# Kernel tuning notes

Hardware: AMD Instinct MI355X
Metric: run time of the kernel (lower is better)

Reference implementation:

```python
import jax, jax.numpy as jnp
import numpy as np

N_NODES = 100000
DROP_P = 0.2


def _degree_norm(idx, n):
    deg = jax.ops.segment_sum(jnp.ones_like(idx, dtype=jnp.float32), idx, num_segments=n)
    return jnp.maximum(deg, 1.0) ** -0.5


def gcn_layer(x, src, dst, W, b, n):
    # DGL GraphConv, norm='both', in_feats > out_feats so weight is applied first.
    norm_src = _degree_norm(src, n)  # out-degree^{-1/2}
    norm_dst = _degree_norm(dst, n)  # in-degree^{-1/2}
    h = (x * norm_src[:, None]) @ W            # [N, d_out]
    agg = jax.ops.segment_sum(h[src], dst, num_segments=n)  # gather-scatter over edges
    return agg * norm_dst[:, None] + b


def setup_inputs() -> dict:
    key = jax.random.key(0)
    k = jax.random.split(key, 5)
    x = jax.random.normal(k[0], (N_NODES, 256), dtype=jnp.float32)
    edge_index = jax.random.randint(k[1], (2, 1600000), 0, N_NODES, dtype=jnp.int64)
    W1 = jax.random.normal(k[2], (256, 128), dtype=jnp.float32) * (1.0 / np.sqrt(256))
    b1 = jnp.zeros((128,), dtype=jnp.float32)
    W2 = jax.random.normal(k[3], (128, 47), dtype=jnp.float32) * (1.0 / np.sqrt(128))
    b2 = jnp.zeros((47,), dtype=jnp.float32)
    return {"x": x, "edge_index": edge_index, "W1": W1, "b1": b1, "W2": W2, "b2": b2}


def reference(x, edge_index, W1, b1, W2, b2):
    src, dst = edge_index[0], edge_index[1]
    n = x.shape[0]
    # CRD: GraphConv -> relu -> dropout (F.dropout default training=True; fixed mask)
    h = gcn_layer(x, src, dst, W1, b1, n)
    h = jax.nn.relu(h)
    keep = jax.random.bernoulli(jax.random.key(42), 1.0 - DROP_P, h.shape)
    h = jnp.where(keep, h / (1.0 - DROP_P), 0.0)
    # CLS: GraphConv -> log_softmax over class dim
    out = gcn_layer(h, src, dst, W2, b2, n)
    return jax.nn.log_softmax(out, axis=-1)
```

## Files before the change

kernel.cpp:

```cpp
#include <hip/hip_runtime.h>
#include <math.h>


#define NF0 256
#define NF1 128
#define NC  47
#define CB  1024

typedef __attribute__((ext_vector_type(8))) short bfrag;
typedef __attribute__((ext_vector_type(4))) float f32x4;

__device__ __forceinline__ unsigned short f2bf(float f) {
  unsigned u = __float_as_uint(f);
  return (unsigned short)((u + 0x7fffu + ((u >> 16) & 1u)) >> 16);
}
__device__ __forceinline__ unsigned pack2bf(float a, float b) {
  return (unsigned)f2bf(a) | ((unsigned)f2bf(b) << 16);
}
__device__ __forceinline__ float bf2f(unsigned short b) {
  return __uint_as_float((unsigned)b << 16);
}
__device__ __forceinline__ float bflo(unsigned v) { return __uint_as_float(v << 16); }
__device__ __forceinline__ float bfhi(unsigned v) { return __uint_as_float(v & 0xffff0000u); }

__device__ __forceinline__ unsigned rotl_(unsigned x, int n) {
  return (x << n) | (x >> (32 - n));
}
__device__ __forceinline__ void threefry2x32_(unsigned x0, unsigned x1,
                                              unsigned& o0, unsigned& o1) {
  const unsigned k0 = 0u, k1 = 42u;
  const unsigned k2 = k0 ^ k1 ^ 0x1BD11BDAu;
  x0 += k0; x1 += k1;
  x0+=x1; x1=rotl_(x1,13); x1^=x0;
  x0+=x1; x1=rotl_(x1,15); x1^=x0;
  x0+=x1; x1=rotl_(x1,26); x1^=x0;
  x0+=x1; x1=rotl_(x1, 6); x1^=x0;
  x0+=k1; x1+=k2+1u;
  x0+=x1; x1=rotl_(x1,17); x1^=x0;
  x0+=x1; x1=rotl_(x1,29); x1^=x0;
  x0+=x1; x1=rotl_(x1,16); x1^=x0;
  x0+=x1; x1=rotl_(x1,24); x1^=x0;
  x0+=k2; x1+=k0+2u;
  x0+=x1; x1=rotl_(x1,13); x1^=x0;
  x0+=x1; x1=rotl_(x1,15); x1^=x0;
  x0+=x1; x1=rotl_(x1,26); x1^=x0;
  x0+=x1; x1=rotl_(x1, 6); x1^=x0;
  x0+=k0; x1+=k1+3u;
  x0+=x1; x1=rotl_(x1,17); x1^=x0;
  x0+=x1; x1=rotl_(x1,29); x1^=x0;
  x0+=x1; x1=rotl_(x1,16); x1^=x0;
  x0+=x1; x1=rotl_(x1,24); x1^=x0;
  x0+=k1; x1+=k2+4u;
  x0+=x1; x1=rotl_(x1,13); x1^=x0;
  x0+=x1; x1=rotl_(x1,15); x1^=x0;
  x0+=x1; x1=rotl_(x1,26); x1^=x0;
  x0+=x1; x1=rotl_(x1, 6); x1^=x0;
  x0+=k2; x1+=k0+5u;
  o0 = x0; o1 = x1;
}
__device__ __forceinline__ float dropout_mul(int j) {
  unsigned o0, o1;
  threefry2x32_(0u, (unsigned)j, o0, o1);
  unsigned bits = o0 ^ o1;
  float u = __uint_as_float((bits >> 9) | 0x3f800000u) - 1.0f;
  return (u < 0.8f) ? 1.25f : 0.0f;
}


__global__ __launch_bounds__(256) void k_chist(const int* __restrict__ ei, int E,
                                               int nbk,
                                               unsigned* __restrict__ bCntD,
                                               unsigned* __restrict__ bCntS) {
  __shared__ unsigned hd[128], hs[128];
  for (int i = threadIdx.x; i < 128; i += 256) { hd[i] = 0; hs[i] = 0; }
  __syncthreads();
  for (int e = blockIdx.x * 256 + threadIdx.x; e < E; e += gridDim.x * 256) {
    int s = ei[e], d = ei[E + e];
    atomicAdd(&hs[s >> 10], 1u);
    atomicAdd(&hd[d >> 10], 1u);
  }
  __syncthreads();
  for (int i = threadIdx.x; i < nbk; i += 256) {
    if (hd[i]) atomicAdd(&bCntD[i], hd[i]);
    if (hs[i]) atomicAdd(&bCntS[i], hs[i]);
  }
}

__global__ void k_cscan(const unsigned* __restrict__ bCntD,
                        const unsigned* __restrict__ bCntS,
                        unsigned* __restrict__ bOffD, unsigned* __restrict__ bOffS,
                        unsigned* __restrict__ curD, unsigned* __restrict__ curS,
                        unsigned* __restrict__ off, int nbk, int N, int E) {
  if (threadIdx.x == 0) {
    unsigned a = 0, b = 0;
    for (int i = 0; i < nbk; i++) {
      bOffD[i] = a; curD[i] = a; a += bCntD[i];
      bOffS[i] = b; curS[i] = b; b += bCntS[i];
    }
    bOffD[nbk] = a; bOffS[nbk] = b;
    off[N] = (unsigned)E;
  }
}

__global__ __launch_bounds__(256) void k_cscatter(const int* __restrict__ ei, int E,
                                                  unsigned* __restrict__ curD,
                                                  unsigned* __restrict__ curS,
                                                  unsigned* __restrict__ pd,
                                                  unsigned short* __restrict__ ps) {
  __shared__ unsigned hd[128], hs[128];
  __shared__ unsigned baseD[128], baseS[128];
  int per = (E + gridDim.x - 1) / gridDim.x;
  int e0 = blockIdx.x * per;
  int e1 = min(e0 + per, E);
  for (int i = threadIdx.x; i < 128; i += 256) { hd[i] = 0; hs[i] = 0; }
  __syncthreads();
  for (int e = e0 + threadIdx.x; e < e1; e += 256) {
    int s = ei[e], d = ei[E + e];
    atomicAdd(&hs[s >> 10], 1u);
    atomicAdd(&hd[d >> 10], 1u);
  }
  __syncthreads();
  for (int i = threadIdx.x; i < 128; i += 256) {
    baseD[i] = hd[i] ? atomicAdd(&curD[i], hd[i]) : 0u;
    baseS[i] = hs[i] ? atomicAdd(&curS[i], hs[i]) : 0u;
    hd[i] = 0; hs[i] = 0;
  }
  __syncthreads();
  for (int e = e0 + threadIdx.x; e < e1; e += 256) {
    int s = ei[e], d = ei[E + e];
    int bd = d >> 10, bs = s >> 10;
    unsigned pD = baseD[bd] + atomicAdd(&hd[bd], 1u);
    unsigned pS = baseS[bs] + atomicAdd(&hs[bs], 1u);
    pd[pD] = ((unsigned)(d & (CB - 1)) << 17) | (unsigned)s;
    ps[pS] = (unsigned short)(s & (CB - 1));
  }
}

__global__ __launch_bounds__(256) void k_fcsr(const unsigned* __restrict__ bOffD,
                                              const unsigned* __restrict__ pd,
                                              unsigned* __restrict__ off,
                                              unsigned* __restrict__ deg_dst, int N,
                                              int* __restrict__ csr) {
  __shared__ unsigned cnt[CB];
  __shared__ unsigned part[256];
  const int b = blockIdx.x, t = threadIdx.x;
  const unsigned lo = bOffD[b], hi = bOffD[b + 1];
  const int base = b << 10;
  for (int i = t; i < CB; i += 256) cnt[i] = 0;
  __syncthreads();
  for (unsigned j = lo + t; j < hi; j += 256) atomicAdd(&cnt[pd[j] >> 17], 1u);
  __syncthreads();
  unsigned c0 = cnt[4*t], c1 = cnt[4*t+1], c2 = cnt[4*t+2], c3 = cnt[4*t+3];
  unsigned tsum = c0 + c1 + c2 + c3;
  part[t] = tsum;
  __syncthreads();
  #pragma unroll
  for (int o = 1; o < 256; o <<= 1) {
    unsigned u = (t >= o) ? part[t - o] : 0u;
    __syncthreads();
    part[t] += u;
    __syncthreads();
  }
  unsigned e0 = part[t] - tsum;
  unsigned p0 = e0, p1 = e0 + c0, p2 = p1 + c1, p3 = p2 + c2;
  int n0 = base + 4 * t;
  if (n0 + 0 < N) { off[n0 + 0] = lo + p0; deg_dst[n0 + 0] = c0; }
  if (n0 + 1 < N) { off[n0 + 1] = lo + p1; deg_dst[n0 + 1] = c1; }
  if (n0 + 2 < N) { off[n0 + 2] = lo + p2; deg_dst[n0 + 2] = c2; }
  if (n0 + 3 < N) { off[n0 + 3] = lo + p3; deg_dst[n0 + 3] = c3; }
  __syncthreads();
  cnt[4*t] = p0; cnt[4*t+1] = p1; cnt[4*t+2] = p2; cnt[4*t+3] = p3;
  __syncthreads();
  for (unsigned j = lo + t; j < hi; j += 256) {
    unsigned v = pd[j];
    unsigned pos = atomicAdd(&cnt[v >> 17], 1u);
    csr[lo + pos] = (int)(v & 0x1FFFFu);
  }
}

__global__ __launch_bounds__(256) void k_fhist(const unsigned* __restrict__ bOffS,
                                               const unsigned short* __restrict__ ps,
                                               unsigned* __restrict__ deg_src, int N) {
  __shared__ unsigned cnt[CB];
  const int b = blockIdx.x, t = threadIdx.x;
  const unsigned lo = bOffS[b], hi = bOffS[b + 1];
  const int base = b << 10;
  for (int i = t; i < CB; i += 256) cnt[i] = 0;
  __syncthreads();
  for (unsigned j = lo + t; j < hi; j += 256) atomicAdd(&cnt[ps[j]], 1u);
  __syncthreads();
  for (int i = t; i < CB; i += 256)
    if (base + i < N) deg_src[base + i] = cnt[i];
}

__global__ __launch_bounds__(256) void k_norm(float* __restrict__ buf, int n2) {
  int i = blockIdx.x * 256 + threadIdx.x;
  if (i < n2) {
    unsigned d = ((const unsigned*)buf)[i];
    float df = (float)(d < 1u ? 1u : d);
    buf[i] = 1.0f / sqrtf(df);
  }
}

__global__ __launch_bounds__(256) void k_wcvt(const float* __restrict__ W1,
                                              const float* __restrict__ W2,
                                              unsigned* __restrict__ W1t32,
                                              unsigned short* __restrict__ W2t) {
  int i = blockIdx.x * 256 + threadIdx.x;
  if (i < 128 * 128) {
    int n = i >> 7, kp = i & 127;
    int k = kp << 1;
    W1t32[i] = pack2bf(W1[(size_t)k * NF1 + n], W1[(size_t)(k + 1) * NF1 + n]);
  } else if (i < 128 * 128 + 48 * 128) {
    int j = i - 128 * 128;
    int f = j >> 7, k = j & 127;
    W2t[j] = (f < NC) ? f2bf(W2[(size_t)k * NC + f]) : (unsigned short)0;
  }
}

__global__ __launch_bounds__(256) void k_gemm1(const float* __restrict__ x,
                                               const unsigned* __restrict__ W1t32,
                                               const float* __restrict__ norm_src,
                                               unsigned short* __restrict__ h1, int N) {
  __shared__ unsigned As[128][20];
  __shared__ unsigned Bs[128][20];
  const int m0 = blockIdx.x * 128;
  const int t = threadIdx.x;
  const int lane = t & 63, wid = t >> 6;
  const int fr = lane & 15, ko = (lane >> 4) * 8;

  f32x4 acc[2][8];
  #pragma unroll
  for (int r = 0; r < 2; r++)
    #pragma unroll
    for (int c = 0; c < 8; c++) acc[r][c] = (f32x4){0.f, 0.f, 0.f, 0.f};

  const int sr = t >> 1;
  const int shw = (t & 1) * 8;

  for (int k0 = 0; k0 < NF0; k0 += 32) {
    {
      unsigned w[8];
      int gm = m0 + sr;
      if (gm < N) {
        const float* p = x + (size_t)gm * NF0 + k0 + shw * 2;
        #pragma unroll
        for (int q = 0; q < 4; q++) {
          float4 v = *(const float4*)(p + q * 4);
          w[2*q]   = pack2bf(v.x, v.y);
          w[2*q+1] = pack2bf(v.z, v.w);
        }
      } else {
        #pragma unroll
        for (int q = 0; q < 8; q++) w[q] = 0u;
      }
      *(uint4*)&As[sr][shw]     = make_uint4(w[0], w[1], w[2], w[3]);
      *(uint4*)&As[sr][shw + 4] = make_uint4(w[4], w[5], w[6], w[7]);
    }
    {
      const unsigned* pb = W1t32 + (size_t)sr * (NF0 / 2) + (k0 >> 1) + shw;
      *(uint4*)&Bs[sr][shw]     = *(const uint4*)pb;
      *(uint4*)&Bs[sr][shw + 4] = *(const uint4*)(pb + 4);
    }
    __syncthreads();
    const unsigned short* As16 = (const unsigned short*)&As[0][0];
    const unsigned short* Bs16 = (const unsigned short*)&Bs[0][0];
    #pragma unroll
    for (int r = 0; r < 2; r++) {
      bfrag a = *(const bfrag*)(As16 + (size_t)(wid * 32 + r * 16 + fr) * 40 + ko);
      #pragma unroll
      for (int c = 0; c < 8; c++) {
        bfrag b = *(const bfrag*)(Bs16 + (size_t)(c * 16 + fr) * 40 + ko);
        acc[r][c] = __builtin_amdgcn_mfma_f32_16x16x32_bf16(a, b, acc[r][c], 0, 0, 0);
      }
    }
    __syncthreads();
  }

  #pragma unroll
  for (int r = 0; r < 2; r++) {
    int rbase = m0 + wid * 32 + r * 16 + (lane >> 4) * 4;
    float ns[4];
    #pragma unroll
    for (int g = 0; g < 4; g++) ns[g] = (rbase + g < N) ? norm_src[rbase + g] : 0.f;
    #pragma unroll
    for (int c = 0; c < 8; c++) {
      int col = c * 16 + fr;
      #pragma unroll
      for (int g = 0; g < 4; g++) {
        int row = rbase + g;
        if (row < N) h1[(size_t)row * NF1 + col] = f2bf(acc[r][c][g] * ns[g]);
      }
    }
  }
}

__global__ __launch_bounds__(256) void k_gather1(const unsigned* __restrict__ off,
                                                 const int* __restrict__ csr,
                                                 const unsigned short* __restrict__ h1,
                                                 const float* __restrict__ norm_dst,
                                                 const float* __restrict__ norm_src,
                                                 const float* __restrict__ b1,
                                                 unsigned short* __restrict__ h2, int N) {
  int node = (blockIdx.x * 256 + threadIdx.x) >> 6;
  int lane = threadIdx.x & 63;
  if (node >= N) return;
  unsigned j = off[node], e1 = off[node + 1];
  int f = lane << 1;
  float ax = 0.f, ay = 0.f;
  for (; j + 4 <= e1; j += 4) {
    int s0 = csr[j], s1 = csr[j+1], s2 = csr[j+2], s3 = csr[j+3];
    unsigned v0 = *(const unsigned*)(h1 + (size_t)s0 * NF1 + f);
    unsigned v1 = *(const unsigned*)(h1 + (size_t)s1 * NF1 + f);
    unsigned v2 = *(const unsigned*)(h1 + (size_t)s2 * NF1 + f);
    unsigned v3 = *(const unsigned*)(h1 + (size_t)s3 * NF1 + f);
    ax += (bflo(v0) + bflo(v1)) + (bflo(v2) + bflo(v3));
    ay += (bfhi(v0) + bfhi(v1)) + (bfhi(v2) + bfhi(v3));
  }
  for (; j < e1; j++) {
    unsigned v = *(const unsigned*)(h1 + (size_t)csr[j] * NF1 + f);
    ax += bflo(v); ay += bfhi(v);
  }
  float nd = norm_dst[node], ns = norm_src[node];
  float2 bb = *(const float2*)(b1 + f);
  float v0 = fmaxf(ax * nd + bb.x, 0.f);
  float v1 = fmaxf(ay * nd + bb.y, 0.f);
  int jf = node * NF1 + f;
  v0 *= dropout_mul(jf) * ns;
  v1 *= dropout_mul(jf + 1) * ns;
  *(unsigned*)(h2 + (size_t)node * NF1 + f) = pack2bf(v0, v1);
}

__global__ __launch_bounds__(256) void k_gemm2(const unsigned short* __restrict__ h2,
                                               const unsigned short* __restrict__ W2t,
                                               unsigned short* __restrict__ g, int N) {
  __shared__ float hs[64][132];
  __shared__ float w2t[48][132];
  const int m0 = blockIdx.x * 64;
  const int t = threadIdx.x;
  #pragma unroll
  for (int l = t; l < 64 * 16; l += 256) {
    int r = l >> 4, c8 = (l & 15) << 3;
    int gm = m0 + r;
    float f[8];
    if (gm < N) {
      uint4 v = *(const uint4*)(h2 + (size_t)gm * NF1 + c8);
      f[0]=bflo(v.x); f[1]=bfhi(v.x); f[2]=bflo(v.y); f[3]=bfhi(v.y);
      f[4]=bflo(v.z); f[5]=bfhi(v.z); f[6]=bflo(v.w); f[7]=bfhi(v.w);
    } else {
      #pragma unroll
      for (int q = 0; q < 8; q++) f[q] = 0.f;
    }
    *(float4*)&hs[r][c8]     = make_float4(f[0], f[1], f[2], f[3]);
    *(float4*)&hs[r][c8 + 4] = make_float4(f[4], f[5], f[6], f[7]);
  }
  for (int l = t; l < 48 * 128; l += 256) {
    int n = l >> 7, k = l & 127;
    w2t[n][k] = bf2f(W2t[l]);
  }
  __syncthreads();
  const int fg = t & 15, mg = t >> 4;
  const int f0 = fg * 3, mt = mg * 4;
  float acc[4][3] = {{0.f}};
  for (int k = 0; k < NF1; k += 4) {
    float4 a[4], b[3];
    #pragma unroll
    for (int i = 0; i < 4; i++) a[i] = *(float4*)&hs[mt + i][k];
    #pragma unroll
    for (int j = 0; j < 3; j++) b[j] = *(float4*)&w2t[f0 + j][k];
    #pragma unroll
    for (int i = 0; i < 4; i++)
      #pragma unroll
      for (int j = 0; j < 3; j++)
        acc[i][j] += a[i].x*b[j].x + a[i].y*b[j].y + a[i].z*b[j].z + a[i].w*b[j].w;
  }
  #pragma unroll
  for (int i = 0; i < 4; i++) {
    int gm = m0 + mt + i;
    if (gm < N) {
      #pragma unroll
      for (int j = 0; j < 3; j++)
        g[(size_t)gm * 48 + f0 + j] = f2bf(acc[i][j]);
    }
  }
}

__global__ __launch_bounds__(256) void k_gather2(const unsigned* __restrict__ off,
                                                 const int* __restrict__ csr,
                                                 const unsigned short* __restrict__ g,
                                                 const float* __restrict__ norm_dst,
                                                 const float* __restrict__ b2,
                                                 float* __restrict__ out, int N) {
  int node = (blockIdx.x * 256 + threadIdx.x) >> 6;
  int lane = threadIdx.x & 63;
  if (node >= N) return;
  unsigned j = off[node], e1 = off[node + 1];
  float acc = 0.f;
  for (; j + 4 <= e1; j += 4) {
    int s0 = csr[j], s1 = csr[j+1], s2 = csr[j+2], s3 = csr[j+3];
    if (lane < 48) {
      float a0 = bf2f(g[(size_t)s0 * 48 + lane]);
      float a1 = bf2f(g[(size_t)s1 * 48 + lane]);
      float a2 = bf2f(g[(size_t)s2 * 48 + lane]);
      float a3 = bf2f(g[(size_t)s3 * 48 + lane]);
      acc += (a0 + a1) + (a2 + a3);
    }
  }
  for (; j < e1; j++) {
    if (lane < 48) acc += bf2f(g[(size_t)csr[j] * 48 + lane]);
  }
  float nd = norm_dst[node];
  float vr = 0.f, m = -INFINITY;
  if (lane < NC) {
    vr = acc * nd + b2[lane];
    m = vr;
  }
  #pragma unroll
  for (int o = 32; o; o >>= 1) m = fmaxf(m, __shfl_xor(m, o));
  float ex = (lane < NC) ? expf(vr - m) : 0.f;
  #pragma unroll
  for (int o = 32; o; o >>= 1) ex += __shfl_xor(ex, o);
  float ls = logf(ex);
  if (lane < NC) out[(size_t)node * NC + lane] = vr - m - ls;
}

extern "C" void kernel_launch(void* const* d_in, const int* in_sizes, int n_in,
                              void* d_out, int out_size, void* d_ws, size_t ws_size,
                              hipStream_t stream) {
  const float* x  = (const float*)d_in[0];
  const int*   ei = (const int*)d_in[1];
  const float* W1 = (const float*)d_in[2];
  const float* b1 = (const float*)d_in[3];
  const float* W2 = (const float*)d_in[4];
  const float* b2 = (const float*)d_in[5];
  float* out = (float*)d_out;

  const int N = in_sizes[0] / NF0;
  const int E = in_sizes[1] / 2;
  const int nbk = (N + CB - 1) / CB;

  unsigned* ws = (unsigned*)d_ws;
  size_t o = 0;
  auto alloc = [&](size_t elems) { size_t p = o; o += (elems + 3) & ~(size_t)3; return p; };
  unsigned* deg_src = ws + alloc(N);
  unsigned* deg_dst = ws + alloc(N);
  unsigned* off     = ws + alloc(N + 1);
  unsigned* bCntD   = ws + alloc(128);
  unsigned* bCntS   = ws + alloc(128);
  unsigned* bOffD   = ws + alloc(132);
  unsigned* bOffS   = ws + alloc(132);
  unsigned* curD    = ws + alloc(128);
  unsigned* curS    = ws + alloc(128);
  unsigned* pd      = ws + alloc(E);
  unsigned short* ps = (unsigned short*)(ws + alloc(E / 2));
  int*      csr     = (int*)(ws + alloc(E));
  unsigned* W1t32   = ws + alloc(128 * 128);
  unsigned short* W2t = (unsigned short*)(ws + alloc(48 * 128 / 2));
  unsigned short* h1  = (unsigned short*)(ws + alloc((size_t)N * NF1 / 2));
  size_t need_h2 = (o + (size_t)N * NF1 / 2) * 4;
  unsigned short* h2 = (ws_size >= need_h2)
                           ? (unsigned short*)(ws + alloc((size_t)N * NF1 / 2))
                           : (unsigned short*)d_in[0];
  unsigned short* g = h1;

  hipMemsetAsync(bCntD, 0, 256 * sizeof(unsigned), stream);

  k_chist<<<256, 256, 0, stream>>>(ei, E, nbk, bCntD, bCntS);
  k_cscan<<<1, 64, 0, stream>>>(bCntD, bCntS, bOffD, bOffS, curD, curS, off, nbk, N, E);
  k_cscatter<<<256, 256, 0, stream>>>(ei, E, curD, curS, pd, ps);
  k_fcsr<<<nbk, 256, 0, stream>>>(bOffD, pd, off, deg_dst, N, csr);
  k_fhist<<<nbk, 256, 0, stream>>>(bOffS, ps, deg_src, N);
  k_norm<<<(2 * N + 255) / 256, 256, 0, stream>>>((float*)deg_src, 2 * N);
  k_wcvt<<<(128 * 128 + 48 * 128 + 255) / 256, 256, 0, stream>>>(W1, W2, W1t32, W2t);
  k_gemm1<<<(N + 127) / 128, 256, 0, stream>>>(x, W1t32, (const float*)deg_src, h1, N);
  k_gather1<<<((size_t)N * 64 + 255) / 256, 256, 0, stream>>>(
      off, csr, h1, (const float*)deg_dst, (const float*)deg_src, b1, h2, N);
  k_gemm2<<<(N + 63) / 64, 256, 0, stream>>>(h2, W2t, g, N);
  k_gather2<<<((size_t)N * 64 + 255) / 256, 256, 0, stream>>>(
      off, csr, g, (const float*)deg_dst, b2, out, N);
}
```

Before: 513.2 us.

## Fuse preprocessing kernels and merge layer-1 gather with layer-2 GEMM

```diff
diff --git a/kernel.cpp b/kernel.cpp
--- a/kernel.cpp
+++ b/kernel.cpp
@@ -17,11 +17,11 @@
 __device__ __forceinline__ unsigned pack2bf(float a, float b) {
   return (unsigned)f2bf(a) | ((unsigned)f2bf(b) << 16);
 }
+__device__ __forceinline__ float bflo(unsigned v) { return __uint_as_float(v << 16); }
+__device__ __forceinline__ float bfhi(unsigned v) { return __uint_as_float(v & 0xffff0000u); }
 __device__ __forceinline__ float bf2f(unsigned short b) {
   return __uint_as_float((unsigned)b << 16);
 }
-__device__ __forceinline__ float bflo(unsigned v) { return __uint_as_float(v << 16); }
-__device__ __forceinline__ float bfhi(unsigned v) { return __uint_as_float(v & 0xffff0000u); }
 
 __device__ __forceinline__ unsigned rotl_(unsigned x, int n) {
   return (x << n) | (x >> (32 - n));
@@ -70,11 +70,29 @@
 __global__ __launch_bounds__(256) void k_chist(const int* __restrict__ ei, int E,
                                                int nbk,
                                                unsigned* __restrict__ bCntD,
-                                               unsigned* __restrict__ bCntS) {
+                                               unsigned* __restrict__ bCntS,
+                                               const float* __restrict__ W1,
+                                               const float* __restrict__ W2,
+                                               unsigned* __restrict__ W1t32,
+                                               unsigned* __restrict__ W2t32) {
+  if (blockIdx.x >= 256) {
+    int i = (blockIdx.x - 256) * 256 + threadIdx.x;
+    if (i < 128 * 128) {
+      int n = i >> 7, k = (i & 127) << 1;
+      W1t32[i] = pack2bf(W1[(size_t)k * NF1 + n], W1[(size_t)(k + 1) * NF1 + n]);
+    } else if (i < 128 * 128 + 48 * 64) {
+      int j = i - 128 * 128;
+      int f = j >> 6, k = (j & 63) << 1;
+      float a = (f < NC) ? W2[(size_t)k * NC + f] : 0.f;
+      float c = (f < NC) ? W2[(size_t)(k + 1) * NC + f] : 0.f;
+      W2t32[j] = pack2bf(a, c);
+    }
+    return;
+  }
   __shared__ unsigned hd[128], hs[128];
   for (int i = threadIdx.x; i < 128; i += 256) { hd[i] = 0; hs[i] = 0; }
   __syncthreads();
-  for (int e = blockIdx.x * 256 + threadIdx.x; e < E; e += gridDim.x * 256) {
+  for (int e = blockIdx.x * 256 + threadIdx.x; e < E; e += 256 * 256) {
     int s = ei[e], d = ei[E + e];
     atomicAdd(&hs[s >> 10], 1u);
     atomicAdd(&hd[d >> 10], 1u);
@@ -86,47 +104,53 @@
   }
 }
 
-__global__ void k_cscan(const unsigned* __restrict__ bCntD,
-                        const unsigned* __restrict__ bCntS,
-                        unsigned* __restrict__ bOffD, unsigned* __restrict__ bOffS,
-                        unsigned* __restrict__ curD, unsigned* __restrict__ curS,
-                        unsigned* __restrict__ off, int nbk, int N, int E) {
-  if (threadIdx.x == 0) {
-    unsigned a = 0, b = 0;
-    for (int i = 0; i < nbk; i++) {
-      bOffD[i] = a; curD[i] = a; a += bCntD[i];
-      bOffS[i] = b; curS[i] = b; b += bCntS[i];
-    }
-    bOffD[nbk] = a; bOffS[nbk] = b;
-    off[N] = (unsigned)E;
-  }
-}
-
 __global__ __launch_bounds__(256) void k_cscatter(const int* __restrict__ ei, int E,
+                                                  const unsigned* __restrict__ bCntD,
+                                                  const unsigned* __restrict__ bCntS,
                                                   unsigned* __restrict__ curD,
                                                   unsigned* __restrict__ curS,
                                                   unsigned* __restrict__ pd,
-                                                  unsigned short* __restrict__ ps) {
+                                                  unsigned short* __restrict__ ps,
+                                                  int nbk) {
   __shared__ unsigned hd[128], hs[128];
   __shared__ unsigned baseD[128], baseS[128];
+  __shared__ unsigned sc[256];
+  const int t = threadIdx.x;
   int per = (E + gridDim.x - 1) / gridDim.x;
   int e0 = blockIdx.x * per;
   int e1 = min(e0 + per, E);
-  for (int i = threadIdx.x; i < 128; i += 256) { hd[i] = 0; hs[i] = 0; }
-  __syncthreads();
-  for (int e = e0 + threadIdx.x; e < e1; e += 256) {
+  unsigned orig = (t < 128) ? ((t < nbk) ? bCntD[t] : 0u)
+                            : (((t - 128) < nbk) ? bCntS[t - 128] : 0u);
+  sc[t] = orig;
+  if (t < 128) { hd[t] = 0; hs[t] = 0; }
+  __syncthreads();
+  for (int e = e0 + t; e < e1; e += 256) {
     int s = ei[e], d = ei[E + e];
     atomicAdd(&hs[s >> 10], 1u);
     atomicAdd(&hd[d >> 10], 1u);
   }
   __syncthreads();
-  for (int i = threadIdx.x; i < 128; i += 256) {
-    baseD[i] = hd[i] ? atomicAdd(&curD[i], hd[i]) : 0u;
-    baseS[i] = hs[i] ? atomicAdd(&curS[i], hs[i]) : 0u;
-    hd[i] = 0; hs[i] = 0;
-  }
-  __syncthreads();
-  for (int e = e0 + threadIdx.x; e < e1; e += 256) {
+  #pragma unroll
+  for (int o = 1; o < 128; o <<= 1) {
+    unsigned u = ((t & 127) >= o) ? sc[t - o] : 0u;
+    __syncthreads();
+    sc[t] += u;
+    __syncthreads();
+  }
+  if (t < 128) {
+    unsigned excl = sc[t] - orig;
+    unsigned h = hd[t];
+    baseD[t] = excl + (h ? atomicAdd(&curD[t], h) : 0u);
+    hd[t] = 0;
+  } else {
+    int i = t - 128;
+    unsigned excl = sc[t] - orig;
+    unsigned h = hs[i];
+    baseS[i] = excl + (h ? atomicAdd(&curS[i], h) : 0u);
+    hs[i] = 0;
+  }
+  __syncthreads();
+  for (int e = e0 + t; e < e1; e += 256) {
     int s = ei[e], d = ei[E + e];
     int bd = d >> 10, bs = s >> 10;
     unsigned pD = baseD[bd] + atomicAdd(&hd[bd], 1u);
@@ -136,85 +160,78 @@
   }
 }
 
-__global__ __launch_bounds__(256) void k_fcsr(const unsigned* __restrict__ bOffD,
+__global__ __launch_bounds__(256) void k_fine(const unsigned* __restrict__ bCntD,
+                                              const unsigned* __restrict__ bCntS,
                                               const unsigned* __restrict__ pd,
+                                              const unsigned short* __restrict__ ps,
                                               unsigned* __restrict__ off,
-                                              unsigned* __restrict__ deg_dst, int N,
-                                              int* __restrict__ csr) {
+                                              float* __restrict__ norm_dst,
+                                              float* __restrict__ norm_src,
+                                              int* __restrict__ csr,
+                                              int N, int E, int nbk) {
   __shared__ unsigned cnt[CB];
   __shared__ unsigned part[256];
-  const int b = blockIdx.x, t = threadIdx.x;
-  const unsigned lo = bOffD[b], hi = bOffD[b + 1];
+  __shared__ unsigned sc[256];
+  const int t = threadIdx.x;
+  const bool isD = (int)blockIdx.x < nbk;
+  const int b = isD ? (int)blockIdx.x : ((int)blockIdx.x - nbk);
+  unsigned orig = (t < 128) ? ((t < nbk) ? bCntD[t] : 0u)
+                            : (((t - 128) < nbk) ? bCntS[t - 128] : 0u);
+  sc[t] = orig;
+  __syncthreads();
+  #pragma unroll
+  for (int o = 1; o < 128; o <<= 1) {
+    unsigned u = ((t & 127) >= o) ? sc[t - o] : 0u;
+    __syncthreads();
+    sc[t] += u;
+    __syncthreads();
+  }
+  const int idx = isD ? b : (128 + b);
+  const unsigned hi = sc[idx];
+  const unsigned lo = hi - (isD ? bCntD[b] : bCntS[b]);
   const int base = b << 10;
   for (int i = t; i < CB; i += 256) cnt[i] = 0;
   __syncthreads();
-  for (unsigned j = lo + t; j < hi; j += 256) atomicAdd(&cnt[pd[j] >> 17], 1u);
-  __syncthreads();
-  unsigned c0 = cnt[4*t], c1 = cnt[4*t+1], c2 = cnt[4*t+2], c3 = cnt[4*t+3];
-  unsigned tsum = c0 + c1 + c2 + c3;
-  part[t] = tsum;
-  __syncthreads();
-  #pragma unroll
-  for (int o = 1; o < 256; o <<= 1) {
-    unsigned u = (t >= o) ? part[t - o] : 0u;
-    __syncthreads();
-    part[t] += u;
-    __syncthreads();
-  }
-  unsigned e0 = part[t] - tsum;
-  unsigned p0 = e0, p1 = e0 + c0, p2 = p1 + c1, p3 = p2 + c2;
-  int n0 = base + 4 * t;
-  if (n0 + 0 < N) { off[n0 + 0] = lo + p0; deg_dst[n0 + 0] = c0; }
-  if (n0 + 1 < N) { off[n0 + 1] = lo + p1; deg_dst[n0 + 1] = c1; }
-  if (n0 + 2 < N) { off[n0 + 2] = lo + p2; deg_dst[n0 + 2] = c2; }
-  if (n0 + 3 < N) { off[n0 + 3] = lo + p3; deg_dst[n0 + 3] = c3; }
-  __syncthreads();
-  cnt[4*t] = p0; cnt[4*t+1] = p1; cnt[4*t+2] = p2; cnt[4*t+3] = p3;
-  __syncthreads();
-  for (unsigned j = lo + t; j < hi; j += 256) {
-    unsigned v = pd[j];
-    unsigned pos = atomicAdd(&cnt[v >> 17], 1u);
-    csr[lo + pos] = (int)(v & 0x1FFFFu);
-  }
-}
-
-__global__ __launch_bounds__(256) void k_fhist(const unsigned* __restrict__ bOffS,
-                                               const unsigned short* __restrict__ ps,
-                                               unsigned* __restrict__ deg_src, int N) {
-  __shared__ unsigned cnt[CB];
-  const int b = blockIdx.x, t = threadIdx.x;
-  const unsigned lo = bOffS[b], hi = bOffS[b + 1];
-  const int base = b << 10;
-  for (int i = t; i < CB; i += 256) cnt[i] = 0;
-  __syncthreads();
-  for (unsigned j = lo + t; j < hi; j += 256) atomicAdd(&cnt[ps[j]], 1u);
-  __syncthreads();
-  for (int i = t; i < CB; i += 256)
-    if (base + i < N) deg_src[base + i] = cnt[i];
-}
-
-__global__ __launch_bounds__(256) void k_norm(float* __restrict__ buf, int n2) {
-  int i = blockIdx.x * 256 + threadIdx.x;
-  if (i < n2) {
-    unsigned d = ((const unsigned*)buf)[i];
-    float df = (float)(d < 1u ? 1u : d);
-    buf[i] = 1.0f / sqrtf(df);
-  }
-}
-
-__global__ __launch_bounds__(256) void k_wcvt(const float* __restrict__ W1,
-                                              const float* __restrict__ W2,
-                                              unsigned* __restrict__ W1t32,
-                                              unsigned short* __restrict__ W2t) {
-  int i = blockIdx.x * 256 + threadIdx.x;
-  if (i < 128 * 128) {
-    int n = i >> 7, kp = i & 127;
-    int k = kp << 1;
-    W1t32[i] = pack2bf(W1[(size_t)k * NF1 + n], W1[(size_t)(k + 1) * NF1 + n]);
-  } else if (i < 128 * 128 + 48 * 128) {
-    int j = i - 128 * 128;
-    int f = j >> 7, k = j & 127;
-    W2t[j] = (f < NC) ? f2bf(W2[(size_t)k * NC + f]) : (unsigned short)0;
+  if (isD) {
+    for (unsigned j = lo + t; j < hi; j += 256) atomicAdd(&cnt[pd[j] >> 17], 1u);
+    __syncthreads();
+    unsigned c0 = cnt[4*t], c1 = cnt[4*t+1], c2 = cnt[4*t+2], c3 = cnt[4*t+3];
+    unsigned tsum = c0 + c1 + c2 + c3;
+    part[t] = tsum;
+    __syncthreads();
+    #pragma unroll
+    for (int o = 1; o < 256; o <<= 1) {
+      unsigned u = (t >= o) ? part[t - o] : 0u;
+      __syncthreads();
+      part[t] += u;
+      __syncthreads();
+    }
+    unsigned e0 = part[t] - tsum;
+    unsigned p0 = e0, p1 = e0 + c0, p2 = p1 + c1, p3 = p2 + c2;
+    int n0 = base + 4 * t;
+    if (n0 + 0 < N) { off[n0+0] = lo + p0; norm_dst[n0+0] = 1.0f / sqrtf((float)(c0 < 1u ? 1u : c0)); }
+    if (n0 + 1 < N) { off[n0+1] = lo + p1; norm_dst[n0+1] = 1.0f / sqrtf((float)(c1 < 1u ? 1u : c1)); }
+    if (n0 + 2 < N) { off[n0+2] = lo + p2; norm_dst[n0+2] = 1.0f / sqrtf((float)(c2 < 1u ? 1u : c2)); }
+    if (n0 + 3 < N) { off[n0+3] = lo + p3; norm_dst[n0+3] = 1.0f / sqrtf((float)(c3 < 1u ? 1u : c3)); }
+    if (b == nbk - 1 && t == 0) off[N] = (unsigned)E;
+    __syncthreads();
+    cnt[4*t] = p0; cnt[4*t+1] = p1; cnt[4*t+2] = p2; cnt[4*t+3] = p3;
+    __syncthreads();
+    for (unsigned j = lo + t; j < hi; j += 256) {
+      unsigned v = pd[j];
+      unsigned pos = atomicAdd(&cnt[v >> 17], 1u);
+      csr[lo + pos] = (int)(v & 0x1FFFFu);
+    }
+  } else {
+    for (unsigned j = lo + t; j < hi; j += 256) atomicAdd(&cnt[ps[j]], 1u);
+    __syncthreads();
+    for (int i = t; i < CB; i += 256) {
+      int n = base + i;
+      if (n < N) {
+        unsigned c = cnt[i];
+        norm_src[n] = 1.0f / sqrtf((float)(c < 1u ? 1u : c));
+      }
+    }
   }
 }
 
@@ -295,92 +312,83 @@
   }
 }
 
-__global__ __launch_bounds__(256) void k_gather1(const unsigned* __restrict__ off,
-                                                 const int* __restrict__ csr,
-                                                 const unsigned short* __restrict__ h1,
-                                                 const float* __restrict__ norm_dst,
-                                                 const float* __restrict__ norm_src,
-                                                 const float* __restrict__ b1,
-                                                 unsigned short* __restrict__ h2, int N) {
-  int node = (blockIdx.x * 256 + threadIdx.x) >> 6;
-  int lane = threadIdx.x & 63;
-  if (node >= N) return;
-  unsigned j = off[node], e1 = off[node + 1];
-  int f = lane << 1;
-  float ax = 0.f, ay = 0.f;
-  for (; j + 4 <= e1; j += 4) {
-    int s0 = csr[j], s1 = csr[j+1], s2 = csr[j+2], s3 = csr[j+3];
-    unsigned v0 = *(const unsigned*)(h1 + (size_t)s0 * NF1 + f);
-    unsigned v1 = *(const unsigned*)(h1 + (size_t)s1 * NF1 + f);
-    unsigned v2 = *(const unsigned*)(h1 + (size_t)s2 * NF1 + f);
-    unsigned v3 = *(const unsigned*)(h1 + (size_t)s3 * NF1 + f);
-    ax += (bflo(v0) + bflo(v1)) + (bflo(v2) + bflo(v3));
-    ay += (bfhi(v0) + bfhi(v1)) + (bfhi(v2) + bfhi(v3));
-  }
-  for (; j < e1; j++) {
-    unsigned v = *(const unsigned*)(h1 + (size_t)csr[j] * NF1 + f);
-    ax += bflo(v); ay += bfhi(v);
-  }
-  float nd = norm_dst[node], ns = norm_src[node];
-  float2 bb = *(const float2*)(b1 + f);
-  float v0 = fmaxf(ax * nd + bb.x, 0.f);
-  float v1 = fmaxf(ay * nd + bb.y, 0.f);
-  int jf = node * NF1 + f;
-  v0 *= dropout_mul(jf) * ns;
-  v1 *= dropout_mul(jf + 1) * ns;
-  *(unsigned*)(h2 + (size_t)node * NF1 + f) = pack2bf(v0, v1);
-}
-
-__global__ __launch_bounds__(256) void k_gemm2(const unsigned short* __restrict__ h2,
-                                               const unsigned short* __restrict__ W2t,
-                                               unsigned short* __restrict__ g, int N) {
-  __shared__ float hs[64][132];
-  __shared__ float w2t[48][132];
+#define G2PAD 70
+__global__ __launch_bounds__(256) void k_g1g2(const unsigned* __restrict__ off,
+                                              const int* __restrict__ csr,
+                                              const unsigned short* __restrict__ h1,
+                                              const float* __restrict__ norm_dst,
+                                              const float* __restrict__ norm_src,
+                                              const float* __restrict__ b1,
+                                              const unsigned* __restrict__ W2t32,
+                                              unsigned short* __restrict__ g, int N) {
+  __shared__ unsigned hsb[64 * G2PAD];
+  const int t = threadIdx.x;
   const int m0 = blockIdx.x * 64;
-  const int t = threadIdx.x;
-  #pragma unroll
-  for (int l = t; l < 64 * 16; l += 256) {
-    int r = l >> 4, c8 = (l & 15) << 3;
-    int gm = m0 + r;
-    float f[8];
-    if (gm < N) {
-      uint4 v = *(const uint4*)(h2 + (size_t)gm * NF1 + c8);
-      f[0]=bflo(v.x); f[1]=bfhi(v.x); f[2]=bflo(v.y); f[3]=bfhi(v.y);
-      f[4]=bflo(v.z); f[5]=bfhi(v.z); f[6]=bflo(v.w); f[7]=bfhi(v.w);
-    } else {
-      #pragma unroll
-      for (int q = 0; q < 8; q++) f[q] = 0.f;
-    }
-    *(float4*)&hs[r][c8]     = make_float4(f[0], f[1], f[2], f[3]);
-    *(float4*)&hs[r][c8 + 4] = make_float4(f[4], f[5], f[6], f[7]);
-  }
-  for (int l = t; l < 48 * 128; l += 256) {
-    int n = l >> 7, k = l & 127;
-    w2t[n][k] = bf2f(W2t[l]);
-  }
-  __syncthreads();
+  const int lane = t & 63, wid = t >> 6;
+  const int f = lane << 1;
+
+  for (int nn = 0; nn < 16; nn++) {
+    int lrow = wid * 16 + nn;
+    int node = m0 + lrow;
+    if (node >= N) break;
+    unsigned j = off[node], e1 = off[node + 1];
+    float ax = 0.f, ay = 0.f;
+    for (; j + 4 <= e1; j += 4) {
+      int s0 = csr[j], s1 = csr[j+1], s2 = csr[j+2], s3 = csr[j+3];
+      unsigned v0 = *(const unsigned*)(h1 + (size_t)s0 * NF1 + f);
+      unsigned v1 = *(const unsigned*)(h1 + (size_t)s1 * NF1 + f);
+      unsigned v2 = *(const unsigned*)(h1 + (size_t)s2 * NF1 + f);
+      unsigned v3 = *(const unsigned*)(h1 + (size_t)s3 * NF1 + f);
+      ax += (bflo(v0) + bflo(v1)) + (bflo(v2) + bflo(v3));
+      ay += (bfhi(v0) + bfhi(v1)) + (bfhi(v2) + bfhi(v3));
+    }
+    for (; j < e1; j++) {
+      unsigned v = *(const unsigned*)(h1 + (size_t)csr[j] * NF1 + f);
+      ax += bflo(v); ay += bfhi(v);
+    }
+    float nd = norm_dst[node], ns = norm_src[node];
+    float2 bb = *(const float2*)(b1 + f);
+    float v0 = fmaxf(ax * nd + bb.x, 0.f);
+    float v1 = fmaxf(ay * nd + bb.y, 0.f);
+    int jf = node * NF1 + f;
+    v0 *= dropout_mul(jf) * ns;
+    v1 *= dropout_mul(jf + 1) * ns;
+    hsb[lrow * G2PAD + lane] = pack2bf(v0, v1);
+  }
+  __syncthreads();
+
   const int fg = t & 15, mg = t >> 4;
   const int f0 = fg * 3, mt = mg * 4;
   float acc[4][3] = {{0.f}};
   for (int k = 0; k < NF1; k += 4) {
-    float4 a[4], b[3];
-    #pragma unroll
-    for (int i = 0; i < 4; i++) a[i] = *(float4*)&hs[mt + i][k];
-    #pragma unroll
-    for (int j = 0; j < 3; j++) b[j] = *(float4*)&w2t[f0 + j][k];
+    float a[4][4];
+    #pragma unroll
+    for (int i = 0; i < 4; i++) {
+      uint2 u = *(const uint2*)&hsb[(mt + i) * G2PAD + (k >> 1)];
+      a[i][0] = bflo(u.x); a[i][1] = bfhi(u.x);
+      a[i][2] = bflo(u.y); a[i][3] = bfhi(u.y);
+    }
+    float bv[3][4];
+    #pragma unroll
+    for (int jj = 0; jj < 3; jj++) {
+      uint2 u = *(const uint2*)(W2t32 + (size_t)(f0 + jj) * 64 + (k >> 1));
+      bv[jj][0] = bflo(u.x); bv[jj][1] = bfhi(u.x);
+      bv[jj][2] = bflo(u.y); bv[jj][3] = bfhi(u.y);
+    }
     #pragma unroll
     for (int i = 0; i < 4; i++)
       #pragma unroll
-      for (int j = 0; j < 3; j++)
-        acc[i][j] += a[i].x*b[j].x + a[i].y*b[j].y + a[i].z*b[j].z + a[i].w*b[j].w;
+      for (int jj = 0; jj < 3; jj++)
+        acc[i][jj] += a[i][0]*bv[jj][0] + a[i][1]*bv[jj][1]
+                    + a[i][2]*bv[jj][2] + a[i][3]*bv[jj][3];
   }
   #pragma unroll
   for (int i = 0; i < 4; i++) {
     int gm = m0 + mt + i;
     if (gm < N) {
       #pragma unroll
-      for (int j = 0; j < 3; j++)
-        g[(size_t)gm * 48 + f0 + j] = f2bf(acc[i][j]);
+      for (int jj = 0; jj < 3; jj++)
+        g[(size_t)gm * 48 + f0 + jj] = f2bf(acc[i][jj]);
     }
   }
 }
@@ -442,40 +450,36 @@
   unsigned* ws = (unsigned*)d_ws;
   size_t o = 0;
   auto alloc = [&](size_t elems) { size_t p = o; o += (elems + 3) & ~(size_t)3; return p; };
-  unsigned* deg_src = ws + alloc(N);
-  unsigned* deg_dst = ws + alloc(N);
-  unsigned* off     = ws + alloc(N + 1);
-  unsigned* bCntD   = ws + alloc(128);
-  unsigned* bCntS   = ws + alloc(128);
-  unsigned* bOffD   = ws + alloc(132);
-  unsigned* bOffS   = ws + alloc(132);
-  unsigned* curD    = ws + alloc(128);
-  unsigned* curS    = ws + alloc(128);
-  unsigned* pd      = ws + alloc(E);
+  float*    norm_src = (float*)(ws + alloc(N));
+  float*    norm_dst = (float*)(ws + alloc(N));
+  unsigned* off      = ws + alloc(N + 1);
+  unsigned* bCntD    = ws + alloc(128);
+  unsigned* bCntS    = ws + alloc(128);
+  unsigned* curD     = ws + alloc(128);
+  unsigned* curS     = ws + alloc(128);
+  unsigned* pd       = ws + alloc(E);
   unsigned short* ps = (unsigned short*)(ws + alloc(E / 2));
-  int*      csr     = (int*)(ws + alloc(E));
-  unsigned* W1t32   = ws + alloc(128 * 128);
-  unsigned short* W2t = (unsigned short*)(ws + alloc(48 * 128 / 2));
-  unsigned short* h1  = (unsigned short*)(ws + alloc((size_t)N * NF1 / 2));
-  size_t need_h2 = (o + (size_t)N * NF1 / 2) * 4;
-  unsigned short* h2 = (ws_size >= need_h2)
-                           ? (unsigned short*)(ws + alloc((size_t)N * NF1 / 2))
-                           : (unsigned short*)d_in[0];
-  unsigned short* g = h1;
-
-  hipMemsetAsync(bCntD, 0, 256 * sizeof(unsigned), stream);
-
-  k_chist<<<256, 256, 0, stream>>>(ei, E, nbk, bCntD, bCntS);
-  k_cscan<<<1, 64, 0, stream>>>(bCntD, bCntS, bOffD, bOffS, curD, curS, off, nbk, N, E);
-  k_cscatter<<<256, 256, 0, stream>>>(ei, E, curD, curS, pd, ps);
-  k_fcsr<<<nbk, 256, 0, stream>>>(bOffD, pd, off, deg_dst, N, csr);
-  k_fhist<<<nbk, 256, 0, stream>>>(bOffS, ps, deg_src, N);
-  k_norm<<<(2 * N + 255) / 256, 256, 0, stream>>>((float*)deg_src, 2 * N);
-  k_wcvt<<<(128 * 128 + 48 * 128 + 255) / 256, 256, 0, stream>>>(W1, W2, W1t32, W2t);
-  k_gemm1<<<(N + 127) / 128, 256, 0, stream>>>(x, W1t32, (const float*)deg_src, h1, N);
-  k_gather1<<<((size_t)N * 64 + 255) / 256, 256, 0, stream>>>(
-      off, csr, h1, (const float*)deg_dst, (const float*)deg_src, b1, h2, N);
-  k_gemm2<<<(N + 63) / 64, 256, 0, stream>>>(h2, W2t, g, N);
+  int*      csr      = (int*)(ws + alloc(E));
+  unsigned* W1t32    = ws + alloc(128 * 128);
+  unsigned* W2t32    = ws + alloc(48 * 64);
+  unsigned short* h1 = (unsigned short*)(ws + alloc((size_t)N * NF1 / 2));
+  unsigned short* gbuf;
+  if ((size_t)E * 3 >= (size_t)N * 48) {
+    gbuf = (unsigned short*)pd;
+  } else {
+    gbuf = (unsigned short*)(ws + alloc(((size_t)N * 48 + 1) / 2));
+  }
+
+  hipMemsetAsync(bCntD, 0, 512 * sizeof(unsigned), stream);
+
+  int wblk = (128 * 128 + 48 * 64 + 255) / 256;
+  k_chist<<<256 + wblk, 256, 0, stream>>>(ei, E, nbk, bCntD, bCntS, W1, W2, W1t32, W2t32);
+  k_cscatter<<<256, 256, 0, stream>>>(ei, E, bCntD, bCntS, curD, curS, pd, ps, nbk);
+  k_fine<<<2 * nbk, 256, 0, stream>>>(bCntD, bCntS, pd, ps, off, norm_dst, norm_src,
+                                      csr, N, E, nbk);
+  k_gemm1<<<(N + 127) / 128, 256, 0, stream>>>(x, W1t32, norm_src, h1, N);
+  k_g1g2<<<(N + 63) / 64, 256, 0, stream>>>(off, csr, h1, norm_dst, norm_src, b1,
+                                            W2t32, gbuf, N);
   k_gather2<<<((size_t)N * 64 + 255) / 256, 256, 0, stream>>>(
-      off, csr, g, (const float*)deg_dst, b2, out, N);
-}
+      off, csr, gbuf, norm_dst, b2, out, N);
+}
```

Result: no change. 518.4 us (+1.0%).
